# Kernel optimization log

Measured on AMD Instinct MI355X. Metric: run time of the kernel, lower is better.

The kernel has to match this reference:

```python
import jax, jax.numpy as jnp
import numpy as np

B, T, DIN, DOUT = 32, 3136, 192, 384
H, QS, WS = 6, 4, 16            # heads, q_stride, window_size (post-pool)
HD = DOUT // H                   # head_dim = 64
INNER = QS * WS                  # tokens per mask unit before pooling = 64
NW = T // INNER                  # num_windows = 49
MLP_HID = 4 * DOUT
EPS = 1e-5


def layer_norm(x, w, b):
    mu = x.mean(-1, keepdims=True)
    var = ((x - mu) ** 2).mean(-1, keepdims=True)
    return (x - mu) * jax.lax.rsqrt(var + EPS) * w + b


def setup_inputs() -> dict:
    key = jax.random.key(0)
    ks = jax.random.split(key, 16)
    rn = lambda k, shp, fan: jax.random.normal(k, shp, jnp.float32) * (fan ** -0.5)
    return {
        "embeddings": jax.random.normal(ks[0], (B, T, DIN), jnp.float32),
        "norm1_w": jnp.ones((DIN,), jnp.float32),
        "norm1_b": jnp.zeros((DIN,), jnp.float32),
        "w_qkv": rn(ks[1], (3 * DOUT, DIN), DIN),
        "b_qkv": jnp.zeros((3 * DOUT,), jnp.float32),
        "w_attn_proj": rn(ks[2], (DOUT, DOUT), DOUT),
        "b_attn_proj": jnp.zeros((DOUT,), jnp.float32),
        "w_res_proj": rn(ks[3], (DOUT, DIN), DIN),
        "b_res_proj": jnp.zeros((DOUT,), jnp.float32),
        "norm2_w": jnp.ones((DOUT,), jnp.float32),
        "norm2_b": jnp.zeros((DOUT,), jnp.float32),
        "w_fc1": rn(ks[4], (MLP_HID, DOUT), DOUT),
        "b_fc1": jnp.zeros((MLP_HID,), jnp.float32),
        "w_fc2": rn(ks[5], (DOUT, MLP_HID), MLP_HID),
        "b_fc2": jnp.zeros((DOUT,), jnp.float32),
    }


def _block(embeddings, norm1_w, norm1_b, w_qkv, b_qkv, w_attn_proj, b_attn_proj,
           w_res_proj, b_res_proj, norm2_w, norm2_b, w_fc1, b_fc1, w_fc2, b_fc2):
    x = layer_norm(embeddings, norm1_w, norm1_b)                 # [B,T,DIN]

    # residual path: project then do_pool (max over q_stride groups)
    res = x @ w_res_proj.T + b_res_proj                          # [B,T,DOUT]
    res = res.reshape(B, QS, T // QS, DOUT).max(axis=1)          # [B,T/QS,DOUT]

    # mask-unit attention
    qkv = x @ w_qkv.T + b_qkv                                    # [B,T,3*DOUT]
    qkv = qkv.reshape(B, INNER, NW, 3, H, HD)
    qkv = jnp.transpose(qkv, (3, 0, 4, 2, 1, 5))                 # [3,B,H,NW,INNER,HD]
    q, k, v = qkv[0], qkv[1], qkv[2]
    q = q.reshape(B, H, NW, QS, WS, HD).max(axis=3)              # q-pool -> [B,H,NW,WS,HD]
    scale = HD ** -0.5
    attn = jax.nn.softmax(jnp.einsum("bhwqd,bhwkd->bhwqk", q * scale, k), axis=-1)
    out = jnp.einsum("bhwqk,bhwkd->bhwqd", attn, v)              # [B,H,NW,WS,HD]
    out = jnp.transpose(out, (0, 3, 2, 1, 4)).reshape(B, WS * NW, DOUT)
    out = out @ w_attn_proj.T + b_attn_proj

    emb = res + out
    h = layer_norm(emb, norm2_w, norm2_b)
    h = jax.nn.gelu(h @ w_fc1.T + b_fc1, approximate=False)
    emb = emb + (h @ w_fc2.T + b_fc2)
    return emb, attn


def reference(embeddings, norm1_w, norm1_b, w_qkv, b_qkv, w_attn_proj, b_attn_proj,
              w_res_proj, b_res_proj, norm2_w, norm2_b, w_fc1, b_fc1, w_fc2, b_fc2):
    return _block(embeddings, norm1_w, norm1_b, w_qkv, b_qkv, w_attn_proj, b_attn_proj,
                  w_res_proj, b_res_proj, norm2_w, norm2_b, w_fc1, b_fc1, w_fc2, b_fc2)
```

## Files before the change

kernel.cpp:

```cpp
#include <hip/hip_runtime.h>
#include <stdint.h>

typedef __bf16 bf16_t;
typedef __attribute__((ext_vector_type(8))) __bf16 bf16x8;
typedef __attribute__((ext_vector_type(4))) __bf16 bf16x4;
typedef __attribute__((ext_vector_type(4))) float f32x4;

#define NB_ 32
#define NT_ 3136
#define DIN_ 192
#define DOUT_ 384
#define NH_ 6
#define HD_ 64
#define NW_ 49
#define WSZ_ 16
#define TP_ 784
#define MLP_ 1536

__device__ __forceinline__ f32x4 mfma16(bf16x8 a, bf16x8 b, f32x4 c) {
  return __builtin_amdgcn_mfma_f32_16x16x32_bf16(a, b, c, 0, 0, 0);
}

__device__ __forceinline__ void gload_lds16(const bf16_t* g, bf16_t* l) {
  __builtin_amdgcn_global_load_lds(
      (const __attribute__((address_space(1))) void*)((const void*)g),
      (__attribute__((address_space(3))) void*)l, 16, 0, 0);
}

__global__ void cvt_kernel(const float* __restrict__ s0, const float* __restrict__ s1,
                           const float* __restrict__ s2, const float* __restrict__ s3,
                           const float* __restrict__ s4, bf16_t* __restrict__ d0,
                           bf16_t* __restrict__ d1, bf16_t* __restrict__ d2,
                           bf16_t* __restrict__ d3, bf16_t* __restrict__ d4) {
  const int b = blockIdx.x;
  const float* s; bf16_t* d; long off;
  if (b < 108)      { s = s0; d = d0; off = (long)b * 2048; }
  else if (b < 144) { s = s1; d = d1; off = (long)(b - 108) * 2048; }
  else if (b < 216) { s = s2; d = d2; off = (long)(b - 144) * 2048; }
  else if (b < 504) { s = s3; d = d3; off = (long)(b - 216) * 2048; }
  else              { s = s4; d = d4; off = (long)(b - 504) * 2048; }
  off += (long)threadIdx.x * 8;
  const float4 a = *(const float4*)(s + off);
  const float4 c = *(const float4*)(s + off + 4);
  bf16x8 o;
  o[0] = (bf16_t)a.x; o[1] = (bf16_t)a.y; o[2] = (bf16_t)a.z; o[3] = (bf16_t)a.w;
  o[4] = (bf16_t)c.x; o[5] = (bf16_t)c.y; o[6] = (bf16_t)c.z; o[7] = (bf16_t)c.w;
  *(bf16x8*)(d + off) = o;
}

template <int D>
__global__ void ln_f32_kernel(const float* __restrict__ in, const float* __restrict__ w,
                              const float* __restrict__ bvec, bf16_t* __restrict__ out) {
  const int row = blockIdx.x * 4 + (threadIdx.x >> 6);
  const int lane = threadIdx.x & 63;
  constexpr int PER = D / 64;
  const float* x = in + (long)row * D;
  float v[PER];
  float s = 0.f;
#pragma unroll
  for (int i = 0; i < PER; i++) { v[i] = x[lane * PER + i]; s += v[i]; }
#pragma unroll
  for (int off = 1; off < 64; off <<= 1) s += __shfl_xor(s, off);
  const float mu = s * (1.f / D);
  float s2 = 0.f;
#pragma unroll
  for (int i = 0; i < PER; i++) { const float d = v[i] - mu; s2 += d * d; }
#pragma unroll
  for (int off = 1; off < 64; off <<= 1) s2 += __shfl_xor(s2, off);
  const float rstd = rsqrtf(s2 * (1.f / D) + 1e-5f);
  bf16_t* o = out + (long)row * D;
#pragma unroll
  for (int i = 0; i < PER; i++) {
    const int c = lane * PER + i;
    o[c] = (bf16_t)((v[i] - mu) * rstd * w[c] + bvec[c]);
  }
}

template <int D>
__global__ void ln_bf16_kernel(const bf16_t* __restrict__ in, const float* __restrict__ w,
                               const float* __restrict__ bvec, bf16_t* __restrict__ out) {
  const int row = blockIdx.x * 4 + (threadIdx.x >> 6);
  const int lane = threadIdx.x & 63;
  constexpr int PER = D / 64;
  const bf16_t* x = in + (long)row * D;
  float v[PER];
  float s = 0.f;
#pragma unroll
  for (int i = 0; i < PER; i++) { v[i] = (float)x[lane * PER + i]; s += v[i]; }
#pragma unroll
  for (int off = 1; off < 64; off <<= 1) s += __shfl_xor(s, off);
  const float mu = s * (1.f / D);
  float s2 = 0.f;
#pragma unroll
  for (int i = 0; i < PER; i++) { const float d = v[i] - mu; s2 += d * d; }
#pragma unroll
  for (int off = 1; off < 64; off <<= 1) s2 += __shfl_xor(s2, off);
  const float rstd = rsqrtf(s2 * (1.f / D) + 1e-5f);
  bf16_t* o = out + (long)row * D;
#pragma unroll
  for (int i = 0; i < PER; i++) {
    const int c = lane * PER + i;
    o[c] = (bf16_t)((v[i] - mu) * rstd * w[c] + bvec[c]);
  }
}

template <int ACT, int HASRES, int POOL, int OF32, int RF32, int BM>
__global__ __launch_bounds__(256) void gemm_t(
    const bf16_t* __restrict__ A, const bf16_t* __restrict__ W,
    const float* __restrict__ bias, const void* __restrict__ resv,
    void* __restrict__ Cv, int M, int N, int K) {
  constexpr int PA = BM / 32;
  constexpr int ABYTES = BM * 128;
  constexpr int BUFSZ = ABYTES + 128 * 128;
  __shared__ __align__(16) char LDSB[2 * BUFSZ];

  const int nwg = gridDim.x;
  const int q = nwg >> 3, rm = nwg & 7;
  const int xcd = blockIdx.x & 7, idx = blockIdx.x >> 3;
  const int wg = (xcd < rm ? xcd * (q + 1) : rm * (q + 1) + (xcd - rm) * q) + idx;

  const int nbn = N >> 7;
  const int bmi = wg / nbn;
  const int bni = wg - bmi * nbn;
  const int m0 = bmi * BM, n0 = bni << 7;
  const int tid = threadIdx.x;
  const int lane = tid & 63;
  const int wid = tid >> 6;
  const int wr = (wid >> 1) * (BM / 2), wc = (wid & 1) * 64;
  const int l15 = lane & 15;
  const int lkb = (lane >> 4) << 4;
  const int srow = tid >> 3;
  const int scolsw = ((tid & 7) << 3) ^ ((srow & 7) << 3);
  const int swzr = (l15 & 7) << 4;

  f32x4 acc[PA][4];
  const f32x4 zero = {0.f, 0.f, 0.f, 0.f};
#pragma unroll
  for (int i = 0; i < PA; i++)
#pragma unroll
    for (int j = 0; j < 4; j++) acc[i][j] = zero;

  long arow[PA];
#pragma unroll
  for (int p = 0; p < PA; p++) {
    const int m = m0 + srow + p * 32;
    if constexpr (POOL) {
      const int b = m / NT_;
      const int mm = m - b * NT_;
      arow[p] = (long)b * NT_ + (mm & 3) * TP_ + (mm >> 2);
    } else {
      arow[p] = m;
    }
  }
  long wrow[4];
#pragma unroll
  for (int p = 0; p < 4; p++) wrow[p] = (long)(n0 + srow + p * 32);

  auto stage = [&](int buf, int k0) {
    char* base = LDSB + buf * BUFSZ;
#pragma unroll
    for (int p = 0; p < PA; p++)
      gload_lds16(A + arow[p] * K + k0 + scolsw, (bf16_t*)(base + p * 4096 + tid * 16));
#pragma unroll
    for (int p = 0; p < 4; p++)
      gload_lds16(W + wrow[p] * K + k0 + scolsw,
                  (bf16_t*)(base + ABYTES + p * 4096 + tid * 16));
  };

  const int nt = K >> 6;
  stage(0, 0);
  int cur = 0;
  for (int t = 0; t < nt; t++) {
    __syncthreads();
    if (t + 1 < nt) stage(cur ^ 1, (t + 1) << 6);
    const char* base = LDSB + cur * BUFSZ;
#pragma unroll
    for (int kk = 0; kk < 2; kk++) {
      bf16x8 af[PA], wf[4];
#pragma unroll
      for (int i = 0; i < PA; i++)
        af[i] = *(const bf16x8*)(base + (wr + i * 16 + l15) * 128 + ((kk * 64 + lkb) ^ swzr));
#pragma unroll
      for (int j = 0; j < 4; j++)
        wf[j] = *(const bf16x8*)(base + ABYTES + (wc + j * 16 + l15) * 128 +
                                 ((kk * 64 + lkb) ^ swzr));
#pragma unroll
      for (int i = 0; i < PA; i++)
#pragma unroll
        for (int j = 0; j < 4; j++) {
          if constexpr (POOL) acc[i][j] = mfma16(af[i], wf[j], acc[i][j]);
          else                acc[i][j] = mfma16(wf[j], af[i], acc[i][j]);
        }
    }
    cur ^= 1;
  }

  const int rg = (lane >> 4) * 4;
  if constexpr (POOL) {
#pragma unroll
    for (int j = 0; j < 4; j++) {
      const int gn = n0 + wc + j * 16 + l15;
      const float bv = bias[gn];
#pragma unroll
      for (int i = 0; i < PA; i++) {
        const float v = fmaxf(fmaxf(acc[i][j][0], acc[i][j][1]),
                              fmaxf(acc[i][j][2], acc[i][j][3])) + bv;
        const long pm = (long)((m0 + wr + i * 16 + rg) >> 2);
        ((bf16_t*)Cv)[pm * N + gn] = (bf16_t)v;
      }
    }
  } else {
#pragma unroll
    for (int i = 0; i < PA; i++) {
      const long gm = m0 + wr + i * 16 + l15;
#pragma unroll
      for (int j = 0; j < 4; j++) {
        const int gn = n0 + wc + j * 16 + rg;
        const float4 bv = *(const float4*)(bias + gn);
        float v[4] = {acc[i][j][0] + bv.x, acc[i][j][1] + bv.y,
                      acc[i][j][2] + bv.z, acc[i][j][3] + bv.w};
        if constexpr (ACT == 1) {
#pragma unroll
          for (int r = 0; r < 4; r++) {
            const float t2 = 1.5957691216f * (v[r] + 0.044715f * v[r] * v[r] * v[r]);
            v[r] = v[r] * (1.f - 1.f / (1.f + __expf(t2)));
          }
        }
        if constexpr (HASRES) {
          if constexpr (RF32) {
            const float4 rv = *(const float4*)((const float*)resv + gm * N + gn);
            v[0] += rv.x; v[1] += rv.y; v[2] += rv.z; v[3] += rv.w;
          } else {
            const bf16x4 rv = *(const bf16x4*)((const bf16_t*)resv + gm * N + gn);
#pragma unroll
            for (int r = 0; r < 4; r++) v[r] += (float)rv[r];
          }
        }
        if constexpr (OF32) {
          float4 o = {v[0], v[1], v[2], v[3]};
          *(float4*)((float*)Cv + gm * N + gn) = o;
        } else {
          bf16x4 o;
#pragma unroll
          for (int r = 0; r < 4; r++) o[r] = (bf16_t)v[r];
          *(bf16x4*)((bf16_t*)Cv + gm * N + gn) = o;
        }
      }
    }
  }
}

__global__ __launch_bounds__(256) void attn_kernel(const bf16_t* __restrict__ qkv,
                                                   float* __restrict__ attn_out,
                                                   bf16_t* __restrict__ obuf) {
  __shared__ __align__(16) bf16_t Vs[4][64 * 64];
  __shared__ __align__(16) bf16_t Ps[4][16 * 64];
  const int wid = threadIdx.x >> 6;
  const int lane = threadIdx.x & 63;
  const int flat = blockIdx.x * 4 + wid;
  const int w = flat % NW_;
  const int h = (flat / NW_) % NH_;
  const int b = flat / (NW_ * NH_);
  const int l15 = lane & 15, lk8 = (lane >> 4) * 8;
  const bf16_t* qb = qkv + (long)b * NT_ * (3 * DOUT_);
  bf16_t* Vw = Vs[wid];
  bf16_t* Pw = Ps[wid];

#pragma unroll
  for (int p = 0; p < 8; p++) {
    const int inner = p * 8 + (lane >> 3);
    const int col = (lane & 7) * 8;
    const bf16x8 t =
        *(const bf16x8*)(qb + (long)(inner * NW_ + w) * (3 * DOUT_) + 2 * DOUT_ + h * HD_ + col);
    *(bf16x8*)&Vw[p * 512 + lane * 8] = t;
  }

  bf16x8 aq[2];
#pragma unroll
  for (int kc = 0; kc < 2; kc++) {
    const int d = kc * 32 + lk8;
    float qv[8];
#pragma unroll
    for (int e = 0; e < 8; e++) qv[e] = -1e30f;
#pragma unroll
    for (int qs = 0; qs < 4; qs++) {
      const bf16x8 t =
          *(const bf16x8*)(qb + (long)((qs * 16 + l15) * NW_ + w) * (3 * DOUT_) + h * HD_ + d);
#pragma unroll
      for (int e = 0; e < 8; e++) qv[e] = fmaxf(qv[e], (float)t[e]);
    }
    bf16x8 a;
#pragma unroll
    for (int e = 0; e < 8; e++) a[e] = (bf16_t)(qv[e] * 0.125f);
    aq[kc] = a;
  }

  f32x4 s4[4];
  const f32x4 zero = {0.f, 0.f, 0.f, 0.f};
#pragma unroll
  for (int nc = 0; nc < 4; nc++) s4[nc] = zero;
#pragma unroll
  for (int nc = 0; nc < 4; nc++) {
#pragma unroll
    for (int kc = 0; kc < 2; kc++) {
      const int tok = nc * 16 + l15;
      const int d = kc * 32 + lk8;
      const bf16x8 bk =
          *(const bf16x8*)(qb + (long)(tok * NW_ + w) * (3 * DOUT_) + DOUT_ + h * HD_ + d);
      s4[nc] = mfma16(aq[kc], bk, s4[nc]);
    }
  }

#pragma unroll
  for (int r = 0; r < 4; r++) {
    float mx = fmaxf(fmaxf(s4[0][r], s4[1][r]), fmaxf(s4[2][r], s4[3][r]));
#pragma unroll
    for (int off = 1; off < 16; off <<= 1) mx = fmaxf(mx, __shfl_xor(mx, off));
    float sm = 0.f;
#pragma unroll
    for (int nc = 0; nc < 4; nc++) {
      const float p = __expf(s4[nc][r] - mx);
      s4[nc][r] = p;
      sm += p;
    }
#pragma unroll
    for (int off = 1; off < 16; off <<= 1) sm += __shfl_xor(sm, off);
    const float inv = 1.f / sm;
#pragma unroll
    for (int nc = 0; nc < 4; nc++) s4[nc][r] *= inv;
  }

  const int rg = (lane >> 4) * 4;
  float* aout = attn_out + (long)flat * (WSZ_ * 64);
#pragma unroll
  for (int nc = 0; nc < 4; nc++) {
#pragma unroll
    for (int r = 0; r < 4; r++) {
      const int row = rg + r, col = nc * 16 + l15;
      aout[row * 64 + col] = s4[nc][r];
      Pw[row * 64 + col] = (bf16_t)s4[nc][r];
    }
  }

  bf16x8 ap[2];
#pragma unroll
  for (int kc = 0; kc < 2; kc++) ap[kc] = *(const bf16x8*)&Pw[l15 * 64 + kc * 32 + lk8];

  f32x4 o4[4];
#pragma unroll
  for (int nc = 0; nc < 4; nc++) o4[nc] = zero;
#pragma unroll
  for (int nc = 0; nc < 4; nc++) {
#pragma unroll
    for (int kc = 0; kc < 2; kc++) {
      bf16x8 bv;
#pragma unroll
      for (int e = 0; e < 8; e++) bv[e] = Vw[(kc * 32 + lk8 + e) * 64 + nc * 16 + l15];
      o4[nc] = mfma16(ap[kc], bv, o4[nc]);
    }
  }

  bf16_t* ob = obuf + (long)b * TP_ * DOUT_;
#pragma unroll
  for (int nc = 0; nc < 4; nc++) {
#pragma unroll
    for (int r = 0; r < 4; r++) {
      const int wsr = rg + r;
      const int tprime = wsr * NW_ + w;
      const int chan = h * HD_ + nc * 16 + l15;
      ob[(long)tprime * DOUT_ + chan] = (bf16_t)o4[nc][r];
    }
  }
}

extern "C" void kernel_launch(void* const* d_in, const int* in_sizes, int n_in,
                              void* d_out, int out_size, void* d_ws, size_t ws_size,
                              hipStream_t stream) {
  const float* emb   = (const float*)d_in[0];
  const float* n1w   = (const float*)d_in[1];
  const float* n1b   = (const float*)d_in[2];
  const float* wqkv  = (const float*)d_in[3];
  const float* bqkv  = (const float*)d_in[4];
  const float* wproj = (const float*)d_in[5];
  const float* bproj = (const float*)d_in[6];
  const float* wres  = (const float*)d_in[7];
  const float* bres  = (const float*)d_in[8];
  const float* n2w   = (const float*)d_in[9];
  const float* n2b   = (const float*)d_in[10];
  const float* wfc1  = (const float*)d_in[11];
  const float* bfc1  = (const float*)d_in[12];
  const float* wfc2  = (const float*)d_in[13];
  const float* bfc2  = (const float*)d_in[14];
  float* out = (float*)d_out;

  const int BT = NB_ * NT_;
  const int BTP = NB_ * TP_;
  const int BSL = 8;
  const int MSL = BSL * NT_;

  char* wsb = (char*)d_ws;
  bf16_t* qkvb = (bf16_t*)(wsb);
  bf16_t* h1   = (bf16_t*)(wsb);
  bf16_t* obuf = (bf16_t*)(wsb + 57802752L);
  bf16_t* resp = (bf16_t*)(wsb + 77070336L);
  bf16_t* h0   = resp;
  bf16_t* emb1 = (bf16_t*)(wsb + 96337920L);
  bf16_t* wbqkv = (bf16_t*)(wsb + 115605504L);
  bf16_t* wbres = wbqkv + 221184L;
  bf16_t* wbproj = wbres + 73728L;
  bf16_t* wbfc1 = wbproj + 147456L;
  bf16_t* wbfc2 = wbfc1 + 589824L;
  float*  prob = out + 9633792L;
  bf16_t* x    = (bf16_t*)(out + 9633792L);

  cvt_kernel<<<792, 256, 0, stream>>>(wqkv, wres, wproj, wfc1, wfc2,
                                      wbqkv, wbres, wbproj, wbfc1, wbfc2);
  ln_f32_kernel<DIN_><<<BT / 4, 256, 0, stream>>>(emb, n1w, n1b, x);
  gemm_t<0, 0, 1, 0, 0, 128><<<(BT / 128) * (DOUT_ / 128), 256, 0, stream>>>(
      x, wbres, bres, nullptr, resp, BT, DOUT_, DIN_);
  for (int s = 0; s < 4; s++) {
    gemm_t<0, 0, 0, 0, 0, 128><<<(MSL / 128) * (3 * DOUT_ / 128), 256, 0, stream>>>(
        x + (long)s * MSL * DIN_, wbqkv, bqkv, nullptr, qkvb, MSL, 3 * DOUT_, DIN_);
    attn_kernel<<<BSL * NH_ * NW_ / 4, 256, 0, stream>>>(
        qkvb, prob + (long)s * 2408448L, obuf + (long)s * 2408448L);
  }
  gemm_t<0, 1, 0, 0, 0, 64><<<(BTP / 64) * (DOUT_ / 128), 256, 0, stream>>>(
      obuf, wbproj, bproj, resp, emb1, BTP, DOUT_, DOUT_);
  ln_bf16_kernel<DOUT_><<<BTP / 4, 256, 0, stream>>>(emb1, n2w, n2b, h0);
  gemm_t<1, 0, 0, 0, 0, 128><<<(BTP / 128) * (MLP_ / 128), 256, 0, stream>>>(
      h0, wbfc1, bfc1, nullptr, h1, BTP, MLP_, DOUT_);
  gemm_t<0, 1, 0, 1, 0, 64><<<(BTP / 64) * (DOUT_ / 128), 256, 0, stream>>>(
      h1, wbfc2, bfc2, emb1, out, BTP, DOUT_, MLP_);
}
```

Baseline: 384.4 us.

## Add 256x128-tile 512-thread GEMM for residual, QKV and FC1 projections

```diff
diff --git a/kernel.cpp b/kernel.cpp
--- a/kernel.cpp
+++ b/kernel.cpp
@@ -104,6 +104,139 @@
   }
 }
 
+template <int ACT, int HASRES, int POOL, int OF32, int RF32>
+__global__ __launch_bounds__(512, 4) void gemm8(
+    const bf16_t* __restrict__ A, const bf16_t* __restrict__ W,
+    const float* __restrict__ bias, const void* __restrict__ resv,
+    void* __restrict__ Cv, int M, int N, int K) {
+  __shared__ __align__(16) char AsB[256 * 128];
+  __shared__ __align__(16) char WsB[128 * 128];
+
+  const int nwg = gridDim.x;
+  const int q = nwg >> 3, rm = nwg & 7;
+  const int xcd = blockIdx.x & 7, idx = blockIdx.x >> 3;
+  const int wg = (xcd < rm ? xcd * (q + 1) : rm * (q + 1) + (xcd - rm) * q) + idx;
+
+  const int nbn = N >> 7;
+  const int bmi = wg / nbn;
+  const int bni = wg - bmi * nbn;
+  const int m0 = bmi << 8, n0 = bni << 7;
+  const int tid = threadIdx.x;
+  const int lane = tid & 63;
+  const int wid = tid >> 6;
+  const int wr = (wid >> 1) * 64, wc = (wid & 1) * 64;
+  const int l15 = lane & 15;
+  const int lkb = (lane >> 4) << 4;
+  const int srow = tid >> 3;
+  const int scolsw = ((tid & 7) << 3) ^ ((srow & 7) << 3);
+  const int swzr = (l15 & 7) << 4;
+
+  f32x4 acc[4][4];
+  const f32x4 zero = {0.f, 0.f, 0.f, 0.f};
+#pragma unroll
+  for (int i = 0; i < 4; i++)
+#pragma unroll
+    for (int j = 0; j < 4; j++) acc[i][j] = zero;
+
+  long arow[4];
+#pragma unroll
+  for (int p = 0; p < 4; p++) {
+    const int m = m0 + p * 64 + srow;
+    if constexpr (POOL) {
+      const int b = m / NT_;
+      const int mm = m - b * NT_;
+      arow[p] = (long)b * NT_ + (mm & 3) * TP_ + (mm >> 2);
+    } else {
+      arow[p] = m;
+    }
+  }
+  long wrow[2];
+#pragma unroll
+  for (int p = 0; p < 2; p++) wrow[p] = (long)(n0 + p * 64 + srow);
+
+  for (int k0 = 0; k0 < K; k0 += 64) {
+    __syncthreads();
+#pragma unroll
+    for (int p = 0; p < 4; p++)
+      gload_lds16(A + arow[p] * K + k0 + scolsw, (bf16_t*)(AsB + p * 8192 + tid * 16));
+#pragma unroll
+    for (int p = 0; p < 2; p++)
+      gload_lds16(W + wrow[p] * K + k0 + scolsw, (bf16_t*)(WsB + p * 8192 + tid * 16));
+    __syncthreads();
+#pragma unroll
+    for (int kk = 0; kk < 2; kk++) {
+      bf16x8 af[4], wf[4];
+#pragma unroll
+      for (int i = 0; i < 4; i++)
+        af[i] = *(const bf16x8*)(AsB + (wr + i * 16 + l15) * 128 + ((kk * 64 + lkb) ^ swzr));
+#pragma unroll
+      for (int j = 0; j < 4; j++)
+        wf[j] = *(const bf16x8*)(WsB + (wc + j * 16 + l15) * 128 + ((kk * 64 + lkb) ^ swzr));
+#pragma unroll
+      for (int i = 0; i < 4; i++)
+#pragma unroll
+        for (int j = 0; j < 4; j++) {
+          if constexpr (POOL) acc[i][j] = mfma16(af[i], wf[j], acc[i][j]);
+          else                acc[i][j] = mfma16(wf[j], af[i], acc[i][j]);
+        }
+    }
+  }
+
+  const int rg = (lane >> 4) * 4;
+  if constexpr (POOL) {
+#pragma unroll
+    for (int j = 0; j < 4; j++) {
+      const int gn = n0 + wc + j * 16 + l15;
+      const float bv = bias[gn];
+#pragma unroll
+      for (int i = 0; i < 4; i++) {
+        const float v = fmaxf(fmaxf(acc[i][j][0], acc[i][j][1]),
+                              fmaxf(acc[i][j][2], acc[i][j][3])) + bv;
+        const long pm = (long)((m0 + wr + i * 16 + rg) >> 2);
+        ((bf16_t*)Cv)[pm * N + gn] = (bf16_t)v;
+      }
+    }
+  } else {
+#pragma unroll
+    for (int i = 0; i < 4; i++) {
+      const long gm = m0 + wr + i * 16 + l15;
+#pragma unroll
+      for (int j = 0; j < 4; j++) {
+        const int gn = n0 + wc + j * 16 + rg;
+        const float4 bv = *(const float4*)(bias + gn);
+        float v[4] = {acc[i][j][0] + bv.x, acc[i][j][1] + bv.y,
+                      acc[i][j][2] + bv.z, acc[i][j][3] + bv.w};
+        if constexpr (ACT == 1) {
+#pragma unroll
+          for (int r = 0; r < 4; r++) {
+            const float t2 = 1.5957691216f * (v[r] + 0.044715f * v[r] * v[r] * v[r]);
+            v[r] = v[r] * (1.f - 1.f / (1.f + __expf(t2)));
+          }
+        }
+        if constexpr (HASRES) {
+          if constexpr (RF32) {
+            const float4 rv = *(const float4*)((const float*)resv + gm * N + gn);
+            v[0] += rv.x; v[1] += rv.y; v[2] += rv.z; v[3] += rv.w;
+          } else {
+            const bf16x4 rv = *(const bf16x4*)((const bf16_t*)resv + gm * N + gn);
+#pragma unroll
+            for (int r = 0; r < 4; r++) v[r] += (float)rv[r];
+          }
+        }
+        if constexpr (OF32) {
+          float4 o = {v[0], v[1], v[2], v[3]};
+          *(float4*)((float*)Cv + gm * N + gn) = o;
+        } else {
+          bf16x4 o;
+#pragma unroll
+          for (int r = 0; r < 4; r++) o[r] = (bf16_t)v[r];
+          *(bf16x4*)((bf16_t*)Cv + gm * N + gn) = o;
+        }
+      }
+    }
+  }
+}
+
 template <int ACT, int HASRES, int POOL, int OF32, int RF32, int BM>
 __global__ __launch_bounds__(256) void gemm_t(
     const bf16_t* __restrict__ A, const bf16_t* __restrict__ W,
@@ -416,10 +549,10 @@
   cvt_kernel<<<792, 256, 0, stream>>>(wqkv, wres, wproj, wfc1, wfc2,
                                       wbqkv, wbres, wbproj, wbfc1, wbfc2);
   ln_f32_kernel<DIN_><<<BT / 4, 256, 0, stream>>>(emb, n1w, n1b, x);
-  gemm_t<0, 0, 1, 0, 0, 128><<<(BT / 128) * (DOUT_ / 128), 256, 0, stream>>>(
+  gemm8<0, 0, 1, 0, 0><<<(BT / 256) * (DOUT_ / 128), 512, 0, stream>>>(
       x, wbres, bres, nullptr, resp, BT, DOUT_, DIN_);
   for (int s = 0; s < 4; s++) {
-    gemm_t<0, 0, 0, 0, 0, 128><<<(MSL / 128) * (3 * DOUT_ / 128), 256, 0, stream>>>(
+    gemm8<0, 0, 0, 0, 0><<<(MSL / 256) * (3 * DOUT_ / 128), 512, 0, stream>>>(
         x + (long)s * MSL * DIN_, wbqkv, bqkv, nullptr, qkvb, MSL, 3 * DOUT_, DIN_);
     attn_kernel<<<BSL * NH_ * NW_ / 4, 256, 0, stream>>>(
         qkvb, prob + (long)s * 2408448L, obuf + (long)s * 2408448L);
@@ -427,7 +560,7 @@
   gemm_t<0, 1, 0, 0, 0, 64><<<(BTP / 64) * (DOUT_ / 128), 256, 0, stream>>>(
       obuf, wbproj, bproj, resp, emb1, BTP, DOUT_, DOUT_);
   ln_bf16_kernel<DOUT_><<<BTP / 4, 256, 0, stream>>>(emb1, n2w, n2b, h0);
-  gemm_t<1, 0, 0, 0, 0, 128><<<(BTP / 128) * (MLP_ / 128), 256, 0, stream>>>(
+  gemm8<1, 0, 0, 0, 0><<<(BTP / 256) * (MLP_ / 128), 512, 0, stream>>>(
       h0, wbfc1, bfc1, nullptr, h1, BTP, MLP_, DOUT_);
   gemm_t<0, 1, 0, 1, 0, 64><<<(BTP / 64) * (DOUT_ / 128), 256, 0, stream>>>(
       h1, wbfc2, bfc2, emb1, out, BTP, DOUT_, MLP_);
```

Measured after the change: 384.9 us. Within noise of the previous version (+0.1%).
